# Optimization experiments

Measured on AMD Instinct MI355X. Metric: run time of the kernel, lower is better.

The kernel has to match this reference:

```python
import math
import jax, jax.numpy as jnp
import numpy as np

B, T, C = 2, 2048, 2048
H, G = 16, 4          # n_head, n_group
HKV = H // G          # kv heads
HD = C // H           # head dim = 128

def setup_inputs() -> dict:
    key = jax.random.key(0)
    ks = jax.random.split(key, 4)
    s = 0.02  # realistic init scale
    return {
        "x": jax.random.normal(ks[0], (B, T, C), jnp.float32),
        "Wkv": jax.random.normal(ks[1], (C, 2 * C // G), jnp.float32) * s,
        "bkv": jnp.zeros((2 * C // G,), jnp.float32),
        "Wq": jax.random.normal(ks[2], (C, C), jnp.float32) * s,
        "bq": jnp.zeros((C,), jnp.float32),
        "Wp": jax.random.normal(ks[3], (C, C), jnp.float32) * s,
        "bp": jnp.zeros((C,), jnp.float32),
    }

def _expand_kv(t):
    # (B,T,HKV*HD) -> replicate each kv head G times -> (B,H,T,HD)
    t = t.reshape(B, T, HKV, HD)
    t = jnp.broadcast_to(t[:, :, None], (B, T, G, HKV, HD)).reshape(B, T, H, HD)
    return t.transpose(0, 2, 1, 3)

def reference(x, Wkv, bkv, Wq, bq, Wp, bp):
    kv = x @ Wkv + bkv                      # (B,T,2C/G)
    k, v = jnp.split(kv, 2, axis=-1)
    q = (x @ Wq + bq).reshape(B, T, H, HD).transpose(0, 2, 1, 3)  # (B,H,T,HD)
    k = _expand_kv(k)
    v = _expand_kv(v)
    att = jnp.einsum('bhqd,bhkd->bhqk', q, k) * (1.0 / math.sqrt(HD))
    mask = jnp.tril(jnp.ones((T, T), bool))
    att = jnp.where(mask, att, -jnp.inf)
    att = jax.nn.softmax(att, axis=-1)
    y = jnp.einsum('bhqk,bhkd->bhqd', att, v)
    y = y.transpose(0, 2, 1, 3).reshape(B, T, C)
    return y @ Wp + bp
```

## Files before the change

### kernel.cpp

```cpp
#include <hip/hip_runtime.h>

#define Bv 2
#define Tv 2048
#define Cv 2048
#define Hv 16
#define HKVv 4
#define HDv 128

typedef __attribute__((ext_vector_type(8))) __bf16 bf16x8;
typedef __attribute__((ext_vector_type(4))) float floatx4;

__device__ __forceinline__ unsigned short f2b(float f) {
  unsigned int x = __float_as_uint(f);
  x += 0x7fffu + ((x >> 16) & 1u);
  return (unsigned short)(x >> 16);
}

#define MFMA(a, b, c) __builtin_amdgcn_mfma_f32_16x16x32_bf16((a), (b), (c), 0, 0, 0)

__device__ __forceinline__ void gld_lds16(const void* g, void* l) {
  __builtin_amdgcn_global_load_lds((const __attribute__((address_space(1))) void*)g,
                                   (__attribute__((address_space(3))) void*)l, 16, 0, 0);
}

__global__ void cvt_kernel(const float* __restrict__ src, unsigned short* __restrict__ dst, int n4) {
  int i = blockIdx.x * blockDim.x + threadIdx.x;
  if (i < n4) {
    float4 f = ((const float4*)src)[i];
    ushort4 u;
    u.x = f2b(f.x); u.y = f2b(f.y); u.z = f2b(f.z); u.w = f2b(f.w);
    ((ushort4*)dst)[i] = u;
  }
}

__global__ void tcvt_kernel(const float* __restrict__ src, unsigned short* __restrict__ dst, int K, int N) {
  __shared__ float tile[32][33];
  int k0 = blockIdx.x * 32, n0 = blockIdx.y * 32;
  int tx = threadIdx.x, ty = threadIdx.y;
  for (int i = ty; i < 32; i += 8)
    tile[i][tx] = src[(size_t)(k0 + i) * N + n0 + tx];
  __syncthreads();
  for (int i = ty; i < 32; i += 8)
    dst[(size_t)(n0 + i) * K + k0 + tx] = f2b(tile[tx][i]);
}

__global__ __launch_bounds__(256) void gemm_qkv(
    const unsigned short* __restrict__ xb,
    const unsigned short* __restrict__ wq_t,
    const unsigned short* __restrict__ wkv_t,
    const float* __restrict__ bq, const float* __restrict__ bkv,
    unsigned short* __restrict__ qs,
    unsigned short* __restrict__ ks,
    unsigned short* __restrict__ vs) {
  __shared__ __align__(16) unsigned short Ash[2][128 * 32];
  __shared__ __align__(16) unsigned short Bsh[2][128 * 32];
  int tid = threadIdx.x;
  int wave = tid >> 6, lane = tid & 63;
  int c = lane & 15, quad = lane >> 4;
  int wr = (wave >> 1) * 64, wc = (wave & 1) * 64;
  int m0 = blockIdx.x * 128, n0 = blockIdx.y * 128;
  bool isq = (n0 < 2048);
  const unsigned short* wt = isq ? (wq_t + (size_t)n0 * 2048)
                                 : (wkv_t + (size_t)(n0 - 2048) * 2048);
  floatx4 zero4 = {0.f, 0.f, 0.f, 0.f};
  floatx4 acc[4][4];
#pragma unroll
  for (int i = 0; i < 4; i++)
#pragma unroll
    for (int j = 0; j < 4; j++) acc[i][j] = zero4;

  const unsigned short* Abase = xb + (size_t)m0 * 2048;
  int s0 = wave * 128 + lane, s1 = wave * 128 + 64 + lane;
  int r0 = s0 >> 2, kc0 = (s0 & 3) ^ ((r0 >> 1) & 3);
  int r1 = s1 >> 2, kc1 = (s1 & 3) ^ ((r1 >> 1) & 3);
  int swz3 = quad ^ ((c >> 1) & 3);
  int dA0 = (wave * 128) * 8, dA1 = (wave * 128 + 64) * 8;

  gld_lds16(Abase + (size_t)r0 * 2048 + kc0 * 8, &Ash[0][0] + dA0);
  gld_lds16(Abase + (size_t)r1 * 2048 + kc1 * 8, &Ash[0][0] + dA1);
  gld_lds16(wt + (size_t)r0 * 2048 + kc0 * 8, &Bsh[0][0] + dA0);
  gld_lds16(wt + (size_t)r1 * 2048 + kc1 * 8, &Bsh[0][0] + dA1);
  __syncthreads();

  for (int it = 0; it < 64; it++) {
    int cur = it & 1;
    if (it + 1 < 64) {
      int k1 = (it + 1) * 32;
      gld_lds16(Abase + (size_t)r0 * 2048 + k1 + kc0 * 8, &Ash[cur ^ 1][0] + dA0);
      gld_lds16(Abase + (size_t)r1 * 2048 + k1 + kc1 * 8, &Ash[cur ^ 1][0] + dA1);
      gld_lds16(wt + (size_t)r0 * 2048 + k1 + kc0 * 8, &Bsh[cur ^ 1][0] + dA0);
      gld_lds16(wt + (size_t)r1 * 2048 + k1 + kc1 * 8, &Bsh[cur ^ 1][0] + dA1);
    }
    bf16x8 af[4], bfv[4];
#pragma unroll
    for (int i = 0; i < 4; i++)
      af[i] = *(const bf16x8*)(&Ash[cur][(wr + i * 16 + c) * 32 + swz3 * 8]);
#pragma unroll
    for (int j = 0; j < 4; j++)
      bfv[j] = *(const bf16x8*)(&Bsh[cur][(wc + j * 16 + c) * 32 + swz3 * 8]);
#pragma unroll
    for (int i = 0; i < 4; i++)
#pragma unroll
      for (int j = 0; j < 4; j++)
        acc[i][j] = MFMA(af[i], bfv[j], acc[i][j]);
    __syncthreads();
  }

#pragma unroll
  for (int i = 0; i < 4; i++) {
#pragma unroll
    for (int j = 0; j < 4; j++) {
#pragma unroll
      for (int r = 0; r < 4; r++) {
        int m = m0 + wr + i * 16 + quad * 4 + r;
        int n = n0 + wc + j * 16 + c;
        int bidx = m >> 11, t = m & 2047;
        float val = acc[i][j][r];
        if (isq) {
          val = (val + bq[n]) * 0.08838834764831845f;
          int hh = n >> 7, d = n & 127;
          qs[((size_t)((bidx * Hv + hh) * Tv) + t) * HDv + d] = f2b(val);
        } else {
          int n2 = n - 2048;
          val += bkv[n2];
          if (n2 < 512) {
            int hh = n2 >> 7, d = n2 & 127;
            ks[((size_t)((bidx * HKVv + hh) * Tv) + t) * HDv + d] = f2b(val);
          } else {
            int n3 = n2 - 512;
            int hh = n3 >> 7, d = n3 & 127;
            vs[((size_t)((bidx * HKVv + hh) * HDv) + d) * Tv + t] = f2b(val);
          }
        }
      }
    }
  }
}

__global__ __launch_bounds__(256, 4) void attn_kernel(
    const unsigned short* __restrict__ qs,
    const unsigned short* __restrict__ ks,
    const unsigned short* __restrict__ vs,
    unsigned short* __restrict__ ys) {
  __shared__ __align__(16) unsigned short Ksh[2][32 * 128];
  __shared__ __align__(16) unsigned short Vsh[2][128 * 32];
  __shared__ __align__(16) unsigned short Psh[4][16 * 32];

  int x = blockIdx.x, h = blockIdx.y, b = blockIdx.z;
  int qt = (h & 8) ? (31 - x) : x;
  int hkv = h & (HKVv - 1);
  int tid = threadIdx.x;
  int wave = tid >> 6, lane = tid & 63;
  int c = lane & 15, quad = lane >> 4;
  int q0w = qt * 64 + wave * 16;
  int qrow = q0w + c;
  int swzK = c & 7, swzV = (c >> 1) & 3;

  const unsigned short* qptr = qs + ((size_t)((b * Hv + h) * Tv) + q0w) * HDv;
  const unsigned short* kbase = ks + (size_t)((b * HKVv + hkv) * Tv) * HDv;
  const unsigned short* vbase = vs + (size_t)((b * HKVv + hkv) * HDv) * Tv;

  bf16x8 qf[4];
#pragma unroll
  for (int kc = 0; kc < 4; kc++)
    qf[kc] = *(const bf16x8*)(qptr + (size_t)c * HDv + kc * 32 + quad * 8);

  floatx4 zero4 = {0.f, 0.f, 0.f, 0.f};
  floatx4 o[8];
#pragma unroll
  for (int dt = 0; dt < 8; dt++) o[dt] = zero4;
  float M = -1e30f, L = 0.f;

  unsigned short* Pw = &Psh[wave][0];

  int kOff[2], vOff[2];
#pragma unroll
  for (int i = 0; i < 2; i++) {
    int s = wave * 128 + i * 64 + lane;
    int rk = s >> 4, gk = (s & 15) ^ (rk & 7);
    kOff[i] = rk * 128 + gk * 8;
    int rv = s >> 2, gv = (s & 3) ^ ((rv >> 1) & 3);
    vOff[i] = rv * Tv + gv * 8;
  }
  int ldsBase = (wave * 128) * 8;

  int ntiles = 2 * qt + 2;

#pragma unroll
  for (int i = 0; i < 2; i++) gld_lds16(kbase + kOff[i], &Ksh[0][0] + ldsBase + i * 512);
#pragma unroll
  for (int i = 0; i < 2; i++) gld_lds16(vbase + vOff[i], &Vsh[0][0] + ldsBase + i * 512);
  __syncthreads();

  for (int kt = 0; kt < ntiles; kt++) {
    int kv0 = kt * 32;
    int cur = kt & 1;
    if (kt + 1 < ntiles) {
      int kv1 = (kt + 1) * 32;
#pragma unroll
      for (int i = 0; i < 2; i++)
        gld_lds16(kbase + (size_t)kv1 * 128 + kOff[i], &Ksh[cur ^ 1][0] + ldsBase + i * 512);
#pragma unroll
      for (int i = 0; i < 2; i++)
        gld_lds16(vbase + kv1 + vOff[i], &Vsh[cur ^ 1][0] + ldsBase + i * 512);
    }

    if (kv0 <= q0w + 15) {
      const unsigned short* Kb = &Ksh[cur][0];
      const unsigned short* Vb = &Vsh[cur][0];
      floatx4 st[2] = {zero4, zero4};
#pragma unroll
      for (int kc = 0; kc < 4; kc++) {
#pragma unroll
        for (int sub = 0; sub < 2; sub++) {
          bf16x8 kf = *(const bf16x8*)(&Kb[(sub * 16 + c) * 128 + (((kc * 4 + quad) ^ swzK) * 8)]);
          st[sub] = MFMA(kf, qf[kc], st[sub]);
        }
      }
      if (kv0 + 31 > q0w) {
#pragma unroll
        for (int sub = 0; sub < 2; sub++) {
          int kvb = kv0 + sub * 16 + quad * 4;
#pragma unroll
          for (int r = 0; r < 4; r++)
            if (kvb + r > qrow) st[sub][r] = -1e30f;
        }
      }
      float mx = -1e30f;
#pragma unroll
      for (int sub = 0; sub < 2; sub++)
        mx = fmaxf(mx, fmaxf(fmaxf(st[sub][0], st[sub][1]), fmaxf(st[sub][2], st[sub][3])));
      mx = fmaxf(mx, __shfl_xor(mx, 16));
      mx = fmaxf(mx, __shfl_xor(mx, 32));
      if (!__all(mx <= M + 8.0f)) {
        float Mn = fmaxf(M, mx);
        float al = __expf(M - Mn);
        M = Mn;
        L *= al;
#pragma unroll
        for (int dt = 0; dt < 8; dt++) o[dt] *= al;
      }
      float l = 0.f;
#pragma unroll
      for (int sub = 0; sub < 2; sub++) {
        float p0 = __expf(st[sub][0] - M);
        float p1 = __expf(st[sub][1] - M);
        float p2 = __expf(st[sub][2] - M);
        float p3 = __expf(st[sub][3] - M);
        l += (p0 + p1) + (p2 + p3);
        unsigned int lo = (unsigned int)f2b(p0) | ((unsigned int)f2b(p1) << 16);
        unsigned int hi = (unsigned int)f2b(p2) | ((unsigned int)f2b(p3) << 16);
        int g = (sub * 2 + (quad >> 1)) ^ swzV;
        *(uint2*)(&Pw[c * 32 + g * 8 + (quad & 1) * 4]) = make_uint2(lo, hi);
      }
      l += __shfl_xor(l, 16);
      l += __shfl_xor(l, 32);
      L += l;
      bf16x8 pf = *(const bf16x8*)(&Pw[c * 32 + ((quad ^ swzV) * 8)]);
#pragma unroll
      for (int dt = 0; dt < 8; dt++) {
        bf16x8 vf = *(const bf16x8*)(&Vb[(dt * 16 + c) * 32 + ((quad ^ swzV) * 8)]);
        o[dt] = MFMA(vf, pf, o[dt]);
      }
    }
    __syncthreads();
  }

  float Li = 1.0f / L;
  size_t rowbase = ((size_t)(b * Tv + qrow)) * Cv + h * HDv;
#pragma unroll
  for (int dt = 0; dt < 8; dt++) {
    unsigned int lo = (unsigned int)f2b(o[dt][0] * Li) | ((unsigned int)f2b(o[dt][1] * Li) << 16);
    unsigned int hi2 = (unsigned int)f2b(o[dt][2] * Li) | ((unsigned int)f2b(o[dt][3] * Li) << 16);
    *(uint2*)(&ys[rowbase + dt * 16 + quad * 4]) = make_uint2(lo, hi2);
  }
}

__global__ __launch_bounds__(256) void gemm_proj(
    const unsigned short* __restrict__ ys,
    const unsigned short* __restrict__ wp_t,
    const float* __restrict__ bp,
    float* __restrict__ out) {
  __shared__ __align__(16) unsigned short Ash[2][128 * 32];
  __shared__ __align__(16) unsigned short Bsh[2][128 * 32];
  int tid = threadIdx.x;
  int wave = tid >> 6, lane = tid & 63;
  int c = lane & 15, quad = lane >> 4;
  int wr = (wave >> 1) * 64, wc = (wave & 1) * 64;
  int m0 = blockIdx.x * 128, n0 = blockIdx.y * 128;
  floatx4 zero4 = {0.f, 0.f, 0.f, 0.f};
  floatx4 acc[4][4];
#pragma unroll
  for (int i = 0; i < 4; i++)
#pragma unroll
    for (int j = 0; j < 4; j++) acc[i][j] = zero4;

  const unsigned short* Abase = ys + (size_t)m0 * 2048;
  const unsigned short* Bbase = wp_t + (size_t)n0 * 2048;
  int s0 = wave * 128 + lane, s1 = wave * 128 + 64 + lane;
  int r0 = s0 >> 2, kc0 = (s0 & 3) ^ ((r0 >> 1) & 3);
  int r1 = s1 >> 2, kc1 = (s1 & 3) ^ ((r1 >> 1) & 3);
  int swz3 = quad ^ ((c >> 1) & 3);
  int dA0 = (wave * 128) * 8, dA1 = (wave * 128 + 64) * 8;

  gld_lds16(Abase + (size_t)r0 * 2048 + kc0 * 8, &Ash[0][0] + dA0);
  gld_lds16(Abase + (size_t)r1 * 2048 + kc1 * 8, &Ash[0][0] + dA1);
  gld_lds16(Bbase + (size_t)r0 * 2048 + kc0 * 8, &Bsh[0][0] + dA0);
  gld_lds16(Bbase + (size_t)r1 * 2048 + kc1 * 8, &Bsh[0][0] + dA1);
  __syncthreads();

  for (int it = 0; it < 64; it++) {
    int cur = it & 1;
    if (it + 1 < 64) {
      int k1 = (it + 1) * 32;
      gld_lds16(Abase + (size_t)r0 * 2048 + k1 + kc0 * 8, &Ash[cur ^ 1][0] + dA0);
      gld_lds16(Abase + (size_t)r1 * 2048 + k1 + kc1 * 8, &Ash[cur ^ 1][0] + dA1);
      gld_lds16(Bbase + (size_t)r0 * 2048 + k1 + kc0 * 8, &Bsh[cur ^ 1][0] + dA0);
      gld_lds16(Bbase + (size_t)r1 * 2048 + k1 + kc1 * 8, &Bsh[cur ^ 1][0] + dA1);
    }
    bf16x8 af[4], bfv[4];
#pragma unroll
    for (int i = 0; i < 4; i++)
      af[i] = *(const bf16x8*)(&Ash[cur][(wr + i * 16 + c) * 32 + swz3 * 8]);
#pragma unroll
    for (int j = 0; j < 4; j++)
      bfv[j] = *(const bf16x8*)(&Bsh[cur][(wc + j * 16 + c) * 32 + swz3 * 8]);
#pragma unroll
    for (int i = 0; i < 4; i++)
#pragma unroll
      for (int j = 0; j < 4; j++)
        acc[i][j] = MFMA(af[i], bfv[j], acc[i][j]);
    __syncthreads();
  }

#pragma unroll
  for (int i = 0; i < 4; i++) {
#pragma unroll
    for (int j = 0; j < 4; j++) {
#pragma unroll
      for (int r = 0; r < 4; r++) {
        int m = m0 + wr + i * 16 + quad * 4 + r;
        int n = n0 + wc + j * 16 + c;
        out[(size_t)m * 2048 + n] = acc[i][j][r] + bp[n];
      }
    }
  }
}

extern "C" void kernel_launch(void* const* d_in, const int* in_sizes, int n_in,
                              void* d_out, int out_size, void* d_ws, size_t ws_size,
                              hipStream_t stream) {
  (void)in_sizes; (void)n_in; (void)out_size; (void)ws_size;
  const float* x   = (const float*)d_in[0];
  const float* Wkv = (const float*)d_in[1];
  const float* bkv = (const float*)d_in[2];
  const float* Wq  = (const float*)d_in[3];
  const float* bq  = (const float*)d_in[4];
  const float* Wp  = (const float*)d_in[5];
  const float* bp  = (const float*)d_in[6];
  float* out = (float*)d_out;

  char* ws = (char*)d_ws;
  unsigned short* xb    = (unsigned short*)(ws + 0);
  unsigned short* wq_t  = (unsigned short*)(ws + 16777216);
  unsigned short* wkv_t = (unsigned short*)(ws + 25165824);
  unsigned short* wp_t  = (unsigned short*)(ws + 29360128);
  unsigned short* qs    = (unsigned short*)(ws + 37748736);
  unsigned short* ks    = (unsigned short*)(ws + 54525952);
  unsigned short* vs    = (unsigned short*)(ws + 58720256);
  unsigned short* ysbuf = (unsigned short*)(ws + 62914560);

  cvt_kernel<<<8192, 256, 0, stream>>>(x, xb, 2097152);
  tcvt_kernel<<<dim3(64, 64), dim3(32, 8), 0, stream>>>(Wq, wq_t, 2048, 2048);
  tcvt_kernel<<<dim3(64, 32), dim3(32, 8), 0, stream>>>(Wkv, wkv_t, 2048, 1024);
  tcvt_kernel<<<dim3(64, 64), dim3(32, 8), 0, stream>>>(Wp, wp_t, 2048, 2048);
  gemm_qkv<<<dim3(32, 24), 256, 0, stream>>>(xb, wq_t, wkv_t, bq, bkv, qs, ks, vs);
  attn_kernel<<<dim3(32, 16, 2), 256, 0, stream>>>(qs, ks, vs, ysbuf);
  gemm_proj<<<dim3(32, 16), 256, 0, stream>>>(ysbuf, wp_t, bp, out);
}
```

Measured before the change: 341.4 us.

## Use 128x256 tiles with 8 waves and triple-buffered LDS in both GEMMs

Both projection GEMMs move from 128x128 tiles with 4 waves and double buffering to 128x256 tiles with 8 waves and a 3-stage LDS ring. The per-iteration __syncthreads is replaced by a single vmcnt wait plus barrier, so two K-slices can be in flight while one is consumed. The goal is to hide global-load latency and reuse the A tile across a wider N. In exchange the grid has half as many blocks, which may underfill the CUs for the proj GEMM (256 blocks). The hand-written vmcnt(3) count must also match the three loads issued per stage.

Measured after the change: 399.8 us. 1.17x slower.

```diff
diff --git a/kernel.cpp b/kernel.cpp
--- a/kernel.cpp
+++ b/kernel.cpp
@@ -44,7 +44,15 @@
     dst[(size_t)(n0 + i) * K + k0 + tx] = f2b(tile[tx][i]);
 }
 
-__global__ __launch_bounds__(256) void gemm_qkv(
+
+#define STAGE3(sl, kk)                                             \
+  do {                                                             \
+    gld_lds16(gA + (kk) * 32, &Ash[sl][0] + sA * 8);               \
+    gld_lds16(gB0 + (kk) * 32, &Bsh[sl][0] + sA * 8);              \
+    gld_lds16(gB1 + (kk) * 32, &Bsh[sl][0] + sB1 * 8);             \
+  } while (0)
+
+__global__ __launch_bounds__(512, 2) void gemm_qkv(
     const unsigned short* __restrict__ xb,
     const unsigned short* __restrict__ wq_t,
     const unsigned short* __restrict__ wkv_t,
@@ -52,16 +60,18 @@
     unsigned short* __restrict__ qs,
     unsigned short* __restrict__ ks,
     unsigned short* __restrict__ vs) {
-  __shared__ __align__(16) unsigned short Ash[2][128 * 32];
-  __shared__ __align__(16) unsigned short Bsh[2][128 * 32];
+  __shared__ __align__(16) unsigned short Ash[3][128 * 32];
+  __shared__ __align__(16) unsigned short Bsh[3][256 * 32];
   int tid = threadIdx.x;
   int wave = tid >> 6, lane = tid & 63;
   int c = lane & 15, quad = lane >> 4;
-  int wr = (wave >> 1) * 64, wc = (wave & 1) * 64;
-  int m0 = blockIdx.x * 128, n0 = blockIdx.y * 128;
+  int wr = (wave >> 2) * 64, wc = (wave & 3) * 64;
+  int m0 = blockIdx.x * 128, n0 = blockIdx.y * 256;
   bool isq = (n0 < 2048);
   const unsigned short* wt = isq ? (wq_t + (size_t)n0 * 2048)
                                  : (wkv_t + (size_t)(n0 - 2048) * 2048);
+  const unsigned short* Abase = xb + (size_t)m0 * 2048;
+
   floatx4 zero4 = {0.f, 0.f, 0.f, 0.f};
   floatx4 acc[4][4];
 #pragma unroll
@@ -69,28 +79,24 @@
 #pragma unroll
     for (int j = 0; j < 4; j++) acc[i][j] = zero4;
 
-  const unsigned short* Abase = xb + (size_t)m0 * 2048;
-  int s0 = wave * 128 + lane, s1 = wave * 128 + 64 + lane;
-  int r0 = s0 >> 2, kc0 = (s0 & 3) ^ ((r0 >> 1) & 3);
-  int r1 = s1 >> 2, kc1 = (s1 & 3) ^ ((r1 >> 1) & 3);
+  int sA = tid, rA = sA >> 2, kcA = (sA & 3) ^ ((rA >> 1) & 3);
+  int sB1 = tid + 512;
+  int rB0 = tid >> 2, kcB0 = (tid & 3) ^ ((rB0 >> 1) & 3);
+  int rB1 = sB1 >> 2, kcB1 = (sB1 & 3) ^ ((rB1 >> 1) & 3);
+  const unsigned short* gA = Abase + (size_t)rA * 2048 + kcA * 8;
+  const unsigned short* gB0 = wt + (size_t)rB0 * 2048 + kcB0 * 8;
+  const unsigned short* gB1 = wt + (size_t)rB1 * 2048 + kcB1 * 8;
   int swz3 = quad ^ ((c >> 1) & 3);
-  int dA0 = (wave * 128) * 8, dA1 = (wave * 128 + 64) * 8;
-
-  gld_lds16(Abase + (size_t)r0 * 2048 + kc0 * 8, &Ash[0][0] + dA0);
-  gld_lds16(Abase + (size_t)r1 * 2048 + kc1 * 8, &Ash[0][0] + dA1);
-  gld_lds16(wt + (size_t)r0 * 2048 + kc0 * 8, &Bsh[0][0] + dA0);
-  gld_lds16(wt + (size_t)r1 * 2048 + kc1 * 8, &Bsh[0][0] + dA1);
-  __syncthreads();
-
-  for (int it = 0; it < 64; it++) {
-    int cur = it & 1;
-    if (it + 1 < 64) {
-      int k1 = (it + 1) * 32;
-      gld_lds16(Abase + (size_t)r0 * 2048 + k1 + kc0 * 8, &Ash[cur ^ 1][0] + dA0);
-      gld_lds16(Abase + (size_t)r1 * 2048 + k1 + kc1 * 8, &Ash[cur ^ 1][0] + dA1);
-      gld_lds16(wt + (size_t)r0 * 2048 + k1 + kc0 * 8, &Bsh[cur ^ 1][0] + dA0);
-      gld_lds16(wt + (size_t)r1 * 2048 + k1 + kc1 * 8, &Bsh[cur ^ 1][0] + dA1);
-    }
+
+  STAGE3(0, 0);
+  STAGE3(1, 1);
+
+  int cur = 0;
+  for (int t = 0; t < 63; ++t) {
+    asm volatile("s_waitcnt vmcnt(3)" ::: "memory");
+    __builtin_amdgcn_s_barrier();
+    int nx2 = cur + 2; if (nx2 >= 3) nx2 -= 3;
+    if (t < 62) STAGE3(nx2, t + 2);
     bf16x8 af[4], bfv[4];
 #pragma unroll
     for (int i = 0; i < 4; i++)
@@ -103,7 +109,23 @@
 #pragma unroll
       for (int j = 0; j < 4; j++)
         acc[i][j] = MFMA(af[i], bfv[j], acc[i][j]);
-    __syncthreads();
+    cur = (cur == 2) ? 0 : cur + 1;
+  }
+  asm volatile("s_waitcnt vmcnt(0)" ::: "memory");
+  __builtin_amdgcn_s_barrier();
+  {
+    bf16x8 af[4], bfv[4];
+#pragma unroll
+    for (int i = 0; i < 4; i++)
+      af[i] = *(const bf16x8*)(&Ash[cur][(wr + i * 16 + c) * 32 + swz3 * 8]);
+#pragma unroll
+    for (int j = 0; j < 4; j++)
+      bfv[j] = *(const bf16x8*)(&Bsh[cur][(wc + j * 16 + c) * 32 + swz3 * 8]);
+#pragma unroll
+    for (int i = 0; i < 4; i++)
+#pragma unroll
+      for (int j = 0; j < 4; j++)
+        acc[i][j] = MFMA(af[i], bfv[j], acc[i][j]);
   }
 
 #pragma unroll
@@ -276,18 +298,21 @@
   }
 }
 
-__global__ __launch_bounds__(256) void gemm_proj(
+__global__ __launch_bounds__(512, 2) void gemm_proj(
     const unsigned short* __restrict__ ys,
     const unsigned short* __restrict__ wp_t,
     const float* __restrict__ bp,
     float* __restrict__ out) {
-  __shared__ __align__(16) unsigned short Ash[2][128 * 32];
-  __shared__ __align__(16) unsigned short Bsh[2][128 * 32];
+  __shared__ __align__(16) unsigned short Ash[3][128 * 32];
+  __shared__ __align__(16) unsigned short Bsh[3][256 * 32];
   int tid = threadIdx.x;
   int wave = tid >> 6, lane = tid & 63;
   int c = lane & 15, quad = lane >> 4;
-  int wr = (wave >> 1) * 64, wc = (wave & 1) * 64;
-  int m0 = blockIdx.x * 128, n0 = blockIdx.y * 128;
+  int wr = (wave >> 2) * 64, wc = (wave & 3) * 64;
+  int m0 = blockIdx.x * 128, n0 = blockIdx.y * 256;
+  const unsigned short* Abase = ys + (size_t)m0 * 2048;
+  const unsigned short* wt = wp_t + (size_t)n0 * 2048;
+
   floatx4 zero4 = {0.f, 0.f, 0.f, 0.f};
   floatx4 acc[4][4];
 #pragma unroll
@@ -295,29 +320,24 @@
 #pragma unroll
     for (int j = 0; j < 4; j++) acc[i][j] = zero4;
 
-  const unsigned short* Abase = ys + (size_t)m0 * 2048;
-  const unsigned short* Bbase = wp_t + (size_t)n0 * 2048;
-  int s0 = wave * 128 + lane, s1 = wave * 128 + 64 + lane;
-  int r0 = s0 >> 2, kc0 = (s0 & 3) ^ ((r0 >> 1) & 3);
-  int r1 = s1 >> 2, kc1 = (s1 & 3) ^ ((r1 >> 1) & 3);
+  int sA = tid, rA = sA >> 2, kcA = (sA & 3) ^ ((rA >> 1) & 3);
+  int sB1 = tid + 512;
+  int rB0 = tid >> 2, kcB0 = (tid & 3) ^ ((rB0 >> 1) & 3);
+  int rB1 = sB1 >> 2, kcB1 = (sB1 & 3) ^ ((rB1 >> 1) & 3);
+  const unsigned short* gA = Abase + (size_t)rA * 2048 + kcA * 8;
+  const unsigned short* gB0 = wt + (size_t)rB0 * 2048 + kcB0 * 8;
+  const unsigned short* gB1 = wt + (size_t)rB1 * 2048 + kcB1 * 8;
   int swz3 = quad ^ ((c >> 1) & 3);
-  int dA0 = (wave * 128) * 8, dA1 = (wave * 128 + 64) * 8;
-
-  gld_lds16(Abase + (size_t)r0 * 2048 + kc0 * 8, &Ash[0][0] + dA0);
-  gld_lds16(Abase + (size_t)r1 * 2048 + kc1 * 8, &Ash[0][0] + dA1);
-  gld_lds16(Bbase + (size_t)r0 * 2048 + kc0 * 8, &Bsh[0][0] + dA0);
-  gld_lds16(Bbase + (size_t)r1 * 2048 + kc1 * 8, &Bsh[0][0] + dA1);
-  __syncthreads();
-
-  for (int it = 0; it < 64; it++) {
-    int cur = it & 1;
-    if (it + 1 < 64) {
-      int k1 = (it + 1) * 32;
-      gld_lds16(Abase + (size_t)r0 * 2048 + k1 + kc0 * 8, &Ash[cur ^ 1][0] + dA0);
-      gld_lds16(Abase + (size_t)r1 * 2048 + k1 + kc1 * 8, &Ash[cur ^ 1][0] + dA1);
-      gld_lds16(Bbase + (size_t)r0 * 2048 + k1 + kc0 * 8, &Bsh[cur ^ 1][0] + dA0);
-      gld_lds16(Bbase + (size_t)r1 * 2048 + k1 + kc1 * 8, &Bsh[cur ^ 1][0] + dA1);
-    }
+
+  STAGE3(0, 0);
+  STAGE3(1, 1);
+
+  int cur = 0;
+  for (int t = 0; t < 63; ++t) {
+    asm volatile("s_waitcnt vmcnt(3)" ::: "memory");
+    __builtin_amdgcn_s_barrier();
+    int nx2 = cur + 2; if (nx2 >= 3) nx2 -= 3;
+    if (t < 62) STAGE3(nx2, t + 2);
     bf16x8 af[4], bfv[4];
 #pragma unroll
     for (int i = 0; i < 4; i++)
@@ -330,7 +350,23 @@
 #pragma unroll
       for (int j = 0; j < 4; j++)
         acc[i][j] = MFMA(af[i], bfv[j], acc[i][j]);
-    __syncthreads();
+    cur = (cur == 2) ? 0 : cur + 1;
+  }
+  asm volatile("s_waitcnt vmcnt(0)" ::: "memory");
+  __builtin_amdgcn_s_barrier();
+  {
+    bf16x8 af[4], bfv[4];
+#pragma unroll
+    for (int i = 0; i < 4; i++)
+      af[i] = *(const bf16x8*)(&Ash[cur][(wr + i * 16 + c) * 32 + swz3 * 8]);
+#pragma unroll
+    for (int j = 0; j < 4; j++)
+      bfv[j] = *(const bf16x8*)(&Bsh[cur][(wc + j * 16 + c) * 32 + swz3 * 8]);
+#pragma unroll
+    for (int i = 0; i < 4; i++)
+#pragma unroll
+      for (int j = 0; j < 4; j++)
+        acc[i][j] = MFMA(af[i], bfv[j], acc[i][j]);
   }
 
 #pragma unroll
@@ -374,7 +410,7 @@
   tcvt_kernel<<<dim3(64, 64), dim3(32, 8), 0, stream>>>(Wq, wq_t, 2048, 2048);
   tcvt_kernel<<<dim3(64, 32), dim3(32, 8), 0, stream>>>(Wkv, wkv_t, 2048, 1024);
   tcvt_kernel<<<dim3(64, 64), dim3(32, 8), 0, stream>>>(Wp, wp_t, 2048, 2048);
-  gemm_qkv<<<dim3(32, 24), 256, 0, stream>>>(xb, wq_t, wkv_t, bq, bkv, qs, ks, vs);
+  gemm_qkv<<<dim3(32, 12), 512, 0, stream>>>(xb, wq_t, wkv_t, bq, bkv, qs, ks, vs);
   attn_kernel<<<dim3(32, 16, 2), 256, 0, stream>>>(qs, ks, vs, ysbuf);
-  gemm_proj<<<dim3(32, 16), 256, 0, stream>>>(ysbuf, wp_t, bp, out);
-}
+  gemm_proj<<<dim3(32, 8), 512, 0, stream>>>(ysbuf, wp_t, bp, out);
+}
```
